# Performance work log

Measured on AMD Instinct MI355X. Metric: run time of the kernel, lower is better.

## Reference

```python
import jax, jax.numpy as jnp
import numpy as np

N_NODES = 50000
N_EDGES = 800000
D_IN = 256
D_OUT = 128
EPS = 1e-9


def setup_inputs() -> dict:
    key = jax.random.key(0)
    ks = jax.random.split(key, 6)
    feat = jax.random.normal(ks[0], (N_NODES, D_IN), dtype=jnp.float32)
    edge_row = jax.random.randint(ks[1], (N_EDGES,), 0, N_NODES)
    edge_col = jax.random.randint(ks[2], (N_EDGES,), 0, N_NODES)
    # normalized adjacency values (positive, ~1/degree scale)
    edge_val = jax.random.uniform(ks[3], (N_EDGES,), dtype=jnp.float32) / 16.0
    # xavier_uniform for Linear(dim_in, dim_out) weights, stored as [D_IN, D_OUT]
    limit = float(np.sqrt(6.0 / (D_IN + D_OUT)))
    W0 = jax.random.uniform(ks[4], (D_IN, D_OUT), minval=-limit, maxval=limit, dtype=jnp.float32)
    W1 = jax.random.uniform(ks[5], (D_IN, D_OUT), minval=-limit, maxval=limit, dtype=jnp.float32)
    zeros = jnp.zeros((D_OUT,), dtype=jnp.float32)
    ones = jnp.ones((D_OUT,), dtype=jnp.float32)
    return {
        "feat": feat,
        "W0": W0, "b0": zeros, "scale0": ones, "offset0": zeros,
        "W1": W1, "b1": zeros, "scale1": ones, "offset1": zeros,
        "edge_row": edge_row, "edge_col": edge_col, "edge_val": edge_val,
    }


def _spmm(edge_row, edge_col, edge_val, x):
    # out[r] += val * x[c] for each edge (r, c, val)  -- sparse adj @ x
    msgs = edge_val[:, None] * x[edge_col]  # [E, D]
    return jax.ops.segment_sum(msgs, edge_row, num_segments=N_NODES)


def _feat_trans(x, W, b, scale, offset):
    h = jax.nn.relu(x @ W + b)  # [N, D_OUT]
    mean = jnp.mean(h, axis=1, keepdims=True)
    var = jnp.var(h, axis=1, keepdims=True) + EPS  # unbiased=False (population var)
    return (h - mean) * scale * jax.lax.rsqrt(var) + offset


def reference(feat, W0, b0, scale0, offset0, W1, b1, scale1, offset1,
              edge_row, edge_col, edge_val):
    # non-first-layer path: feat_hop = [X, A @ X] (order=1), dropout p=0 is identity
    hop1 = _spmm(edge_row, edge_col, edge_val, feat)
    f0 = _feat_trans(feat, W0, b0, scale0, offset0)
    f1 = _feat_trans(hop1, W1, b1, scale1, offset1)
    return jnp.concatenate([f0, f1], axis=1)  # aggr == 'concat'
```

## Files before the change

### kernel.cpp

```cpp
#include <hip/hip_runtime.h>

#define N_NODES 50000
#define N_EDGES 800000
#define D_IN    256
#define D_OUT   128
#define EPS     1e-9f
#define BPAD    136

#define SCATTER_BLOCKS 196
#define GEMM_MBLKS     391

#define RPB    64
#define NBUCK  782
#define BCAP   1344
#define GSTR   16
#define LCAP   1792

#define SORT_OFF  0
#define HIST_OFF  32768
#define LOFF_OFF  35896
#define BASE_OFF  39024
#define CSUM_OFF  42152
#define CBAS_OFF  42216
#define SMEM_BYTES 42280

typedef __attribute__((ext_vector_type(8))) short bf16x8;
typedef __attribute__((ext_vector_type(4))) float floatx4;

__device__ __forceinline__ ushort f2bf(float x) {
    unsigned u = __float_as_uint(x);
    u += 0x7fffu + ((u >> 16) & 1u);
    return (ushort)(u >> 16);
}

__device__ __forceinline__ bf16x8 packbf(float4 a, float4 b) {
    union { ushort us[8]; bf16x8 v; } r;
    r.us[0] = f2bf(a.x); r.us[1] = f2bf(a.y);
    r.us[2] = f2bf(a.z); r.us[3] = f2bf(a.w);
    r.us[4] = f2bf(b.x); r.us[5] = f2bf(b.y);
    r.us[6] = f2bf(b.z); r.us[7] = f2bf(b.w);
    return r.v;
}

#define WB_BLOCKS  32
__global__ __launch_bounds__(256) void prep_small(
    const float* __restrict__ W0, const float* __restrict__ W1,
    ushort* __restrict__ Wb, int* __restrict__ gcnt)
{
    int bid = blockIdx.x;
    int t   = threadIdx.x;
    if (bid == 0) {
        for (int i = t; i < NBUCK * GSTR; i += 256) gcnt[i] = 0;
    } else {
        int g  = (bid - 1) * 256 + t;
        int n  = g >> 5;
        int kq = g & 31;
        const float* W = (n < 128) ? W0 : W1;
        int nn = n & 127;
        union { ushort us[8]; uint4 v; } tmp;
#pragma unroll
        for (int j = 0; j < 8; ++j)
            tmp.us[j] = f2bf(W[(size_t)(kq * 8 + j) * D_OUT + nn]);
        *(uint4*)&Wb[(size_t)n * D_IN + kq * 8] = tmp.v;
    }
}

__global__ __launch_bounds__(512, 4) void gemm_scatter(
    const float* __restrict__ feat, const ushort* __restrict__ Wb,
    const float* __restrict__ bias, const float* __restrict__ scale,
    const float* __restrict__ offset,
    float* __restrict__ out, ushort* __restrict__ Y1,
    const int* __restrict__ er, const int* __restrict__ ec,
    const float* __restrict__ ev, int* __restrict__ gcnt,
    uint2* __restrict__ bedge)
{
    __shared__ __align__(16) char smem[SMEM_BYTES];

    const int t = threadIdx.x;

    if (blockIdx.x < SCATTER_BLOCKS) {
        uint2* sorted = (uint2*)(smem + SORT_OFF);
        int*   hist   = (int*)(smem + HIST_OFF);
        int*   loff   = (int*)(smem + LOFF_OFF);
        int*   base   = (int*)(smem + BASE_OFF);
        int*   csum   = (int*)(smem + CSUM_OFF);
        int*   cbas   = (int*)(smem + CBAS_OFF);

        for (int i = t; i < NBUCK; i += 512) hist[i] = 0;
        __syncthreads();

        const int ebase  = blockIdx.x * 4096;
        const int ecount = min(4096, N_EDGES - ebase);
        int   bkt[8], rnk[8];
        uint2 pk[8];
#pragma unroll
        for (int u = 0; u < 8; ++u) {
            int e = ebase + u * 512 + t;
            bool ok = (e < N_EDGES);
            int   r = ok ? er[e] : 0;
            int   c = ok ? ec[e] : 0;
            float v = ok ? ev[e] : 0.f;
            int   b = r >> 6;
            bkt[u] = ok ? b : -1;
            pk[u]  = make_uint2(((unsigned)b << 22) |
                                ((unsigned)(r & 63) << 16) | (unsigned)c,
                                __float_as_uint(v));
            if (ok) rnk[u] = atomicAdd(&hist[b], 1);
        }
        __syncthreads();

        {
            const int lane = t & 63, w = t >> 6;
            int v0 = (t < NBUCK) ? hist[t] : 0;
            int x0 = v0;
#pragma unroll
            for (int s = 1; s < 64; s <<= 1) {
                int y = __shfl_up(x0, s);
                if (lane >= s) x0 += y;
            }
            if (lane == 63) csum[w] = x0;
            const int i1 = t + 512;
            int v1 = (i1 < NBUCK) ? hist[i1] : 0;
            int x1 = v1;
#pragma unroll
            for (int s = 1; s < 64; s <<= 1) {
                int y = __shfl_up(x1, s);
                if (lane >= s) x1 += y;
            }
            if (lane == 63) csum[8 + w] = x1;
            __syncthreads();
            if (t == 0) {
                int run = 0;
#pragma unroll
                for (int c = 0; c < 16; ++c) { cbas[c] = run; run += csum[c]; }
            }
            __syncthreads();
            if (t < NBUCK)  loff[t]  = x0 - v0 + cbas[w];
            if (i1 < NBUCK) loff[i1] = x1 - v1 + cbas[8 + w];
        }
        __syncthreads();

#pragma unroll
        for (int u = 0; u < 8; ++u) {
            if (bkt[u] >= 0)
                sorted[loff[bkt[u]] + rnk[u]] = pk[u];
        }
        for (int i = t; i < NBUCK; i += 512) {
            int h = hist[i];
            base[i] = h ? atomicAdd(&gcnt[i * GSTR], h) : 0;
        }
        __syncthreads();

#pragma unroll
        for (int u = 0; u < 8; ++u) {
            int k = t + u * 512;
            if (k < ecount) {
                uint2 e = sorted[k];
                int b   = (int)(e.x >> 22);
                int pos = base[b] + (k - loff[b]);
                if (pos < BCAP)
                    bedge[(size_t)b * BCAP + pos] = e;
            }
        }
        return;
    }

    const int gbid = blockIdx.x - SCATTER_BLOCKS;
    const int half = gbid / GEMM_MBLKS;
    const int mblk = gbid % GEMM_MBLKS;
    const int wave = t >> 6, lane = t & 63;
    const int quad = lane >> 4, l16 = lane & 15;
    const int m0   = mblk * 128;
    const int n0   = half * 128;
    ushort* Bs = (ushort*)smem;

    const int grow = m0 + wave * 16 + l16;
    const int arow = grow < N_NODES ? grow : 0;
    const float* aptr = &feat[(size_t)arow * D_IN + quad * 8];

    floatx4 acc[8];
#pragma unroll
    for (int nt = 0; nt < 8; ++nt)
        acc[nt] = (floatx4){0.f, 0.f, 0.f, 0.f};

    for (int kt = 0; kt < D_IN; kt += 128) {
#pragma unroll
        for (int i = 0; i < 8; ++i) {
            int g = t + i * 512;
            int row = g >> 4, kq = g & 15;
            *(uint4*)&Bs[row * BPAD + kq * 8] =
                *(const uint4*)&Wb[(size_t)(n0 + row) * D_IN + kt + kq * 8];
        }
        __syncthreads();

        const float* p = aptr + kt;
        float4 q0 = *(const float4*)(p +  0), q1 = *(const float4*)(p +  4);
        float4 q2 = *(const float4*)(p + 32), q3 = *(const float4*)(p + 36);
        float4 q4 = *(const float4*)(p + 64), q5 = *(const float4*)(p + 68);
        float4 q6 = *(const float4*)(p + 96), q7 = *(const float4*)(p + 100);
        bf16x8 a0 = packbf(q0, q1), a1 = packbf(q2, q3);
        bf16x8 a2 = packbf(q4, q5), a3 = packbf(q6, q7);

#pragma unroll
        for (int s = 0; s < 4; ++s) {
            bf16x8 a = (s == 0) ? a0 : (s == 1) ? a1 : (s == 2) ? a2 : a3;
            const int kk = s * 32;
            bf16x8 b[8];
#pragma unroll
            for (int nt = 0; nt < 8; ++nt)
                b[nt] = *(bf16x8*)&Bs[(nt * 16 + l16) * BPAD + kk + quad * 8];
#pragma unroll
            for (int nt = 0; nt < 8; ++nt)
                acc[nt] = __builtin_amdgcn_mfma_f32_16x16x32_bf16(
                    a, b[nt], acc[nt], 0, 0, 0);
        }
        __syncthreads();
    }

    if (half == 0) {
        float bb[8], sc[8], of[8];
#pragma unroll
        for (int nt = 0; nt < 8; ++nt) {
            bb[nt] = bias[nt * 16 + l16];
            sc[nt] = scale[nt * 16 + l16];
            of[nt] = offset[nt * 16 + l16];
        }
#pragma unroll
        for (int i = 0; i < 4; ++i) {
            float h[8], s = 0.f, q = 0.f;
#pragma unroll
            for (int nt = 0; nt < 8; ++nt) {
                h[nt] = fmaxf(acc[nt][i] + bb[nt], 0.f);
                s += h[nt];
                q += h[nt] * h[nt];
            }
#pragma unroll
            for (int m = 1; m < 16; m <<= 1) {
                s += __shfl_xor(s, m);
                q += __shfl_xor(q, m);
            }
            float mean = s * (1.f / 128.f);
            float inv  = rsqrtf(q * (1.f / 128.f) - mean * mean + EPS);
            int row = m0 + wave * 16 + quad * 4 + i;
            if (row < N_NODES) {
#pragma unroll
                for (int nt = 0; nt < 8; ++nt)
                    out[(size_t)row * 256 + nt * 16 + l16] =
                        (h[nt] - mean) * sc[nt] * inv + of[nt];
            }
        }
    } else {
#pragma unroll
        for (int i = 0; i < 4; ++i) {
            int row = m0 + wave * 16 + quad * 4 + i;
            if (row < N_NODES) {
#pragma unroll
                for (int nt = 0; nt < 8; ++nt)
                    Y1[(size_t)row * D_OUT + nt * 16 + l16] =
                        f2bf(acc[nt][i]);
            }
        }
    }
}

__global__ __launch_bounds__(512) void spmm_csr_ln(
    const int* __restrict__ gcnt, const uint2* __restrict__ bedge,
    const ushort* __restrict__ Y,
    const float* __restrict__ bias, const float* __restrict__ scale,
    const float* __restrict__ offset, float* __restrict__ out)
{
    __shared__ uint2 lds_e[LCAP];
    __shared__ int   cnt[RPB];
    __shared__ int   offx[RPB];
    __shared__ int   cntp[RPB];

    const int t      = threadIdx.x;
    const int bucket = blockIdx.x;
    const int r0     = bucket * RPB;
    const int nrows  = min(RPB, N_NODES - r0);
    int ne = gcnt[bucket * GSTR];
    ne = ne < BCAP ? ne : BCAP;

    if (t < RPB) cnt[t] = 0;
    {
        uint4* ez = (uint4*)lds_e;
        ez[t] = make_uint4(0u, 0u, 0u, 0u);
        if (t + 512 < 896) ez[t + 512] = make_uint4(0u, 0u, 0u, 0u);
    }
    __syncthreads();

    const size_t base = (size_t)bucket * BCAP;
    int   erA = -1, erB = -1, erC = -1;
    unsigned exA = 0, exB = 0, exC = 0;
    unsigned evA = 0, evB = 0, evC = 0;
    int   rkA = 0,  rkB = 0,  rkC = 0;
    if (t < ne) {
        uint2 p = bedge[base + t];
        erA = (int)((p.x >> 16) & 63u); exA = (p.x & 0xffffu) << 8;
        evA = p.y;
        rkA = atomicAdd(&cnt[erA], 1);
    }
    if (t + 512 < ne) {
        uint2 p = bedge[base + t + 512];
        erB = (int)((p.x >> 16) & 63u); exB = (p.x & 0xffffu) << 8;
        evB = p.y;
        rkB = atomicAdd(&cnt[erB], 1);
    }
    if (t + 1024 < ne) {
        uint2 p = bedge[base + t + 1024];
        erC = (int)((p.x >> 16) & 63u); exC = (p.x & 0xffffu) << 8;
        evC = p.y;
        rkC = atomicAdd(&cnt[erC], 1);
    }
    __syncthreads();

    if (t < RPB) {
        int c  = cnt[t];
        int cp = (c + 7) & ~7;
        int x  = cp;
#pragma unroll
        for (int s = 1; s < RPB; s <<= 1) {
            int w = __shfl_up(x, s);
            if (t >= s) x += w;
        }
        offx[t] = x - cp;
        cntp[t] = cp;
    }
    __syncthreads();

    if (erA >= 0) lds_e[offx[erA] + rkA] = make_uint2(exA, evA);
    if (erB >= 0) lds_e[offx[erB] + rkB] = make_uint2(exB, evB);
    if (erC >= 0) lds_e[offx[erC] + rkC] = make_uint2(exC, evC);
    __syncthreads();

    const int wave  = t >> 6, lane = t & 63;
    const int lane4 = lane * 4;
    const int cidx  = lane * 2;
    const char* Yb  = (const char*)Y;
    const float b0v = bias[cidx],   b1v = bias[cidx + 1];
    const float s0v = scale[cidx],  s1v = scale[cidx + 1];
    const float o0v = offset[cidx], o1v = offset[cidx + 1];

    for (int ri = wave; ri < nrows; ri += 8) {
        int beg = offx[ri], np = cntp[ri];
        float ax = 0.f, ay = 0.f;
        for (int j = 0; j < np; j += 8) {
            uint2 e[8];
#pragma unroll
            for (int u = 0; u < 8; ++u)
                e[u] = lds_e[beg + j + u];
            unsigned yv[8];
#pragma unroll
            for (int u = 0; u < 8; ++u)
                yv[u] = *(const unsigned*)(Yb + e[u].x + lane4);
#pragma unroll
            for (int u = 0; u < 8; ++u) {
                float v = __uint_as_float(e[u].y);
                ax = fmaf(v, __uint_as_float(yv[u] << 16), ax);
                ay = fmaf(v, __uint_as_float(yv[u] & 0xffff0000u), ay);
            }
        }
        float h0 = fmaxf(ax + b0v, 0.f);
        float h1 = fmaxf(ay + b1v, 0.f);
        float s = h0 + h1, q = h0 * h0 + h1 * h1;
#pragma unroll
        for (int m = 1; m < 64; m <<= 1) {
            s += __shfl_xor(s, m);
            q += __shfl_xor(q, m);
        }
        float mean = s * (1.f / 128.f);
        float inv  = rsqrtf(q * (1.f / 128.f) - mean * mean + EPS);
        int row = r0 + ri;
        float2 o;
        o.x = (h0 - mean) * s0v * inv + o0v;
        o.y = (h1 - mean) * s1v * inv + o1v;
        *(float2*)&out[(size_t)row * 256 + 128 + cidx] = o;
    }
}

extern "C" void kernel_launch(void* const* d_in, const int* in_sizes, int n_in,
                              void* d_out, int out_size, void* d_ws, size_t ws_size,
                              hipStream_t stream)
{
    const float* feat = (const float*)d_in[0];
    const float* W0   = (const float*)d_in[1];
    const float* b0   = (const float*)d_in[2];
    const float* s0   = (const float*)d_in[3];
    const float* o0   = (const float*)d_in[4];
    const float* W1   = (const float*)d_in[5];
    const float* b1   = (const float*)d_in[6];
    const float* s1   = (const float*)d_in[7];
    const float* o1   = (const float*)d_in[8];
    const int*   er   = (const int*)d_in[9];
    const int*   ec   = (const int*)d_in[10];
    const float* ev   = (const float*)d_in[11];
    float* out = (float*)d_out;

    char*   wsb   = (char*)d_ws;
    ushort* Wb    = (ushort*)(wsb);
    ushort* Y1    = (ushort*)(wsb + 131072);
    int*    gcnt  = (int*)   (wsb + 12931072);
    uint2*  bedge = (uint2*) (wsb + 12981248);

    prep_small<<<1 + WB_BLOCKS, 256, 0, stream>>>(W0, W1, Wb, gcnt);

    gemm_scatter<<<SCATTER_BLOCKS + 2 * GEMM_MBLKS, 512, 0, stream>>>(
        feat, Wb, b0, s0, o0, out, Y1, er, ec, ev, gcnt, bedge);

    spmm_csr_ln<<<NBUCK, 512, 0, stream>>>(
        gcnt, bedge, Y1, b1, s1, o1, out);
}
```

Before: 173.9 us.

## Compute both weight halves per GEMM block to reuse feature loads

Each GEMM block now computes all 256 output columns (W0 and W1 halves) for its 128 rows instead of splitting the two halves across separate blocks. The K loop is retiled to 64-wide steps with a smaller LDS stride so both weight halves fit in shared memory. This halves the number of GEMM blocks and stops each feature row from being read and converted to bf16 twice. In exchange, accumulator registers double, which can lower occupancy, and each block carries more serial work.

New measurement: 178.5 us. +2.7%, slower.

```diff
diff --git a/kernel.cpp b/kernel.cpp
--- a/kernel.cpp
+++ b/kernel.cpp
@@ -5,7 +5,7 @@
 #define D_IN    256
 #define D_OUT   128
 #define EPS     1e-9f
-#define BPAD    136
+#define BSTR    72
 
 #define SCATTER_BLOCKS 196
 #define GEMM_MBLKS     391
@@ -165,59 +165,60 @@
         return;
     }
 
-    const int gbid = blockIdx.x - SCATTER_BLOCKS;
-    const int half = gbid / GEMM_MBLKS;
-    const int mblk = gbid % GEMM_MBLKS;
+    const int mblk = blockIdx.x - SCATTER_BLOCKS;
     const int wave = t >> 6, lane = t & 63;
     const int quad = lane >> 4, l16 = lane & 15;
     const int m0   = mblk * 128;
-    const int n0   = half * 128;
     ushort* Bs = (ushort*)smem;
 
     const int grow = m0 + wave * 16 + l16;
     const int arow = grow < N_NODES ? grow : 0;
     const float* aptr = &feat[(size_t)arow * D_IN + quad * 8];
 
-    floatx4 acc[8];
-#pragma unroll
-    for (int nt = 0; nt < 8; ++nt)
+    floatx4 acc[16];
+#pragma unroll
+    for (int nt = 0; nt < 16; ++nt)
         acc[nt] = (floatx4){0.f, 0.f, 0.f, 0.f};
 
-    for (int kt = 0; kt < D_IN; kt += 128) {
-#pragma unroll
-        for (int i = 0; i < 8; ++i) {
+    for (int kt = 0; kt < D_IN; kt += 64) {
+#pragma unroll
+        for (int i = 0; i < 4; ++i) {
             int g = t + i * 512;
-            int row = g >> 4, kq = g & 15;
-            *(uint4*)&Bs[row * BPAD + kq * 8] =
-                *(const uint4*)&Wb[(size_t)(n0 + row) * D_IN + kt + kq * 8];
+            int row = g >> 3, kq = g & 7;
+            *(uint4*)&Bs[row * BSTR + kq * 8] =
+                *(const uint4*)&Wb[(size_t)row * D_IN + kt + kq * 8];
         }
         __syncthreads();
 
         const float* p = aptr + kt;
         float4 q0 = *(const float4*)(p +  0), q1 = *(const float4*)(p +  4);
         float4 q2 = *(const float4*)(p + 32), q3 = *(const float4*)(p + 36);
-        float4 q4 = *(const float4*)(p + 64), q5 = *(const float4*)(p + 68);
-        float4 q6 = *(const float4*)(p + 96), q7 = *(const float4*)(p + 100);
         bf16x8 a0 = packbf(q0, q1), a1 = packbf(q2, q3);
-        bf16x8 a2 = packbf(q4, q5), a3 = packbf(q6, q7);
-
-#pragma unroll
-        for (int s = 0; s < 4; ++s) {
-            bf16x8 a = (s == 0) ? a0 : (s == 1) ? a1 : (s == 2) ? a2 : a3;
+
+#pragma unroll
+        for (int s = 0; s < 2; ++s) {
+            bf16x8 a = s ? a1 : a0;
             const int kk = s * 32;
             bf16x8 b[8];
 #pragma unroll
             for (int nt = 0; nt < 8; ++nt)
-                b[nt] = *(bf16x8*)&Bs[(nt * 16 + l16) * BPAD + kk + quad * 8];
+                b[nt] = *(bf16x8*)&Bs[(nt * 16 + l16) * BSTR + kk + quad * 8];
 #pragma unroll
             for (int nt = 0; nt < 8; ++nt)
                 acc[nt] = __builtin_amdgcn_mfma_f32_16x16x32_bf16(
                     a, b[nt], acc[nt], 0, 0, 0);
-        }
-        __syncthreads();
-    }
-
-    if (half == 0) {
+#pragma unroll
+            for (int nt = 0; nt < 8; ++nt)
+                b[nt] = *(bf16x8*)&Bs[(128 + nt * 16 + l16) * BSTR + kk + quad * 8];
+#pragma unroll
+            for (int nt = 0; nt < 8; ++nt)
+                acc[8 + nt] = __builtin_amdgcn_mfma_f32_16x16x32_bf16(
+                    a, b[nt], acc[8 + nt], 0, 0, 0);
+        }
+        __syncthreads();
+    }
+
+    {
         float bb[8], sc[8], of[8];
 #pragma unroll
         for (int nt = 0; nt < 8; ++nt) {
@@ -247,17 +248,10 @@
                 for (int nt = 0; nt < 8; ++nt)
                     out[(size_t)row * 256 + nt * 16 + l16] =
                         (h[nt] - mean) * sc[nt] * inv + of[nt];
-            }
-        }
-    } else {
-#pragma unroll
-        for (int i = 0; i < 4; ++i) {
-            int row = m0 + wave * 16 + quad * 4 + i;
-            if (row < N_NODES) {
 #pragma unroll
                 for (int nt = 0; nt < 8; ++nt)
                     Y1[(size_t)row * D_OUT + nt * 16 + l16] =
-                        f2bf(acc[nt][i]);
+                        f2bf(acc[8 + nt][i]);
             }
         }
     }
@@ -404,7 +398,7 @@
 
     prep_small<<<1 + WB_BLOCKS, 256, 0, stream>>>(W0, W1, Wb, gcnt);
 
-    gemm_scatter<<<SCATTER_BLOCKS + 2 * GEMM_MBLKS, 512, 0, stream>>>(
+    gemm_scatter<<<SCATTER_BLOCKS + GEMM_MBLKS, 512, 0, stream>>>(
         feat, Wb, b0, s0, o0, out, Y1, er, ec, ev, gcnt, bedge);
 
     spmm_csr_ln<<<NBUCK, 512, 0, stream>>>(
```

## Drop local edge sort in scatter and shrink GEMM LDS tile for occupancy

Applied to the files above, without the earlier changes.

The scatter blocks no longer sort edges in shared memory by bucket. Each thread now writes its edges straight to the global bucket array at base plus its atomic rank, which removes the prefix scan, the sorted staging buffer and several barriers. The GEMM staging of the B tile moves from two 128-wide K phases to four 64-wide phases with a narrower stride, cutting shared memory from about 42KB to about 18.5KB so more blocks can be resident. The cost is scattered, less coalesced global writes for edges and more barriers per K loop in the GEMM.

Measured after the change: 178.9 us. +2.9%, slower.

```diff
diff --git a/kernel.cpp b/kernel.cpp
--- a/kernel.cpp
+++ b/kernel.cpp
@@ -5,7 +5,7 @@
 #define D_IN    256
 #define D_OUT   128
 #define EPS     1e-9f
-#define BPAD    136
+#define BSTR    72
 
 #define SCATTER_BLOCKS 196
 #define GEMM_MBLKS     391
@@ -16,13 +16,9 @@
 #define GSTR   16
 #define LCAP   1792
 
-#define SORT_OFF  0
-#define HIST_OFF  32768
-#define LOFF_OFF  35896
-#define BASE_OFF  39024
-#define CSUM_OFF  42152
-#define CBAS_OFF  42216
-#define SMEM_BYTES 42280
+#define HIST_OFF  0
+#define BASE_OFF  3200
+#define SMEM_BYTES 18560
 
 typedef __attribute__((ext_vector_type(8))) short bf16x8;
 typedef __attribute__((ext_vector_type(4))) float floatx4;
@@ -79,18 +75,12 @@
     const int t = threadIdx.x;
 
     if (blockIdx.x < SCATTER_BLOCKS) {
-        uint2* sorted = (uint2*)(smem + SORT_OFF);
-        int*   hist   = (int*)(smem + HIST_OFF);
-        int*   loff   = (int*)(smem + LOFF_OFF);
-        int*   base   = (int*)(smem + BASE_OFF);
-        int*   csum   = (int*)(smem + CSUM_OFF);
-        int*   cbas   = (int*)(smem + CBAS_OFF);
-
+        int* hist = (int*)(smem + HIST_OFF);
+        int* base = (int*)(smem + BASE_OFF);
         for (int i = t; i < NBUCK; i += 512) hist[i] = 0;
         __syncthreads();
 
-        const int ebase  = blockIdx.x * 4096;
-        const int ecount = min(4096, N_EDGES - ebase);
+        int ebase = blockIdx.x * 4096;
         int   bkt[8], rnk[8];
         uint2 pk[8];
 #pragma unroll
@@ -100,66 +90,23 @@
             int   r = ok ? er[e] : 0;
             int   c = ok ? ec[e] : 0;
             float v = ok ? ev[e] : 0.f;
-            int   b = r >> 6;
-            bkt[u] = ok ? b : -1;
-            pk[u]  = make_uint2(((unsigned)b << 22) |
-                                ((unsigned)(r & 63) << 16) | (unsigned)c,
+            bkt[u] = ok ? (r >> 6) : -1;
+            pk[u]  = make_uint2(((unsigned)(r & 63) << 16) | (unsigned)c,
                                 __float_as_uint(v));
-            if (ok) rnk[u] = atomicAdd(&hist[b], 1);
-        }
-        __syncthreads();
-
-        {
-            const int lane = t & 63, w = t >> 6;
-            int v0 = (t < NBUCK) ? hist[t] : 0;
-            int x0 = v0;
-#pragma unroll
-            for (int s = 1; s < 64; s <<= 1) {
-                int y = __shfl_up(x0, s);
-                if (lane >= s) x0 += y;
-            }
-            if (lane == 63) csum[w] = x0;
-            const int i1 = t + 512;
-            int v1 = (i1 < NBUCK) ? hist[i1] : 0;
-            int x1 = v1;
-#pragma unroll
-            for (int s = 1; s < 64; s <<= 1) {
-                int y = __shfl_up(x1, s);
-                if (lane >= s) x1 += y;
-            }
-            if (lane == 63) csum[8 + w] = x1;
-            __syncthreads();
-            if (t == 0) {
-                int run = 0;
-#pragma unroll
-                for (int c = 0; c < 16; ++c) { cbas[c] = run; run += csum[c]; }
-            }
-            __syncthreads();
-            if (t < NBUCK)  loff[t]  = x0 - v0 + cbas[w];
-            if (i1 < NBUCK) loff[i1] = x1 - v1 + cbas[8 + w];
-        }
-        __syncthreads();
-
-#pragma unroll
-        for (int u = 0; u < 8; ++u) {
-            if (bkt[u] >= 0)
-                sorted[loff[bkt[u]] + rnk[u]] = pk[u];
-        }
+            if (ok) rnk[u] = atomicAdd(&hist[r >> 6], 1);
+        }
+        __syncthreads();
         for (int i = t; i < NBUCK; i += 512) {
             int h = hist[i];
             base[i] = h ? atomicAdd(&gcnt[i * GSTR], h) : 0;
         }
         __syncthreads();
-
 #pragma unroll
         for (int u = 0; u < 8; ++u) {
-            int k = t + u * 512;
-            if (k < ecount) {
-                uint2 e = sorted[k];
-                int b   = (int)(e.x >> 22);
-                int pos = base[b] + (k - loff[b]);
+            if (bkt[u] >= 0) {
+                int pos = base[bkt[u]] + rnk[u];
                 if (pos < BCAP)
-                    bedge[(size_t)b * BCAP + pos] = e;
+                    bedge[(size_t)bkt[u] * BCAP + pos] = pk[u];
             }
         }
         return;
@@ -183,12 +130,14 @@
     for (int nt = 0; nt < 8; ++nt)
         acc[nt] = (floatx4){0.f, 0.f, 0.f, 0.f};
 
-    for (int kt = 0; kt < D_IN; kt += 128) {
-#pragma unroll
-        for (int i = 0; i < 8; ++i) {
+#pragma unroll
+    for (int ph = 0; ph < 4; ++ph) {
+        const int kt = ph * 64;
+#pragma unroll
+        for (int i = 0; i < 2; ++i) {
             int g = t + i * 512;
-            int row = g >> 4, kq = g & 15;
-            *(uint4*)&Bs[row * BPAD + kq * 8] =
+            int row = g >> 3, kq = g & 7;
+            *(uint4*)&Bs[row * BSTR + kq * 8] =
                 *(const uint4*)&Wb[(size_t)(n0 + row) * D_IN + kt + kq * 8];
         }
         __syncthreads();
@@ -196,23 +145,20 @@
         const float* p = aptr + kt;
         float4 q0 = *(const float4*)(p +  0), q1 = *(const float4*)(p +  4);
         float4 q2 = *(const float4*)(p + 32), q3 = *(const float4*)(p + 36);
-        float4 q4 = *(const float4*)(p + 64), q5 = *(const float4*)(p + 68);
-        float4 q6 = *(const float4*)(p + 96), q7 = *(const float4*)(p + 100);
         bf16x8 a0 = packbf(q0, q1), a1 = packbf(q2, q3);
-        bf16x8 a2 = packbf(q4, q5), a3 = packbf(q6, q7);
-
-#pragma unroll
-        for (int s = 0; s < 4; ++s) {
-            bf16x8 a = (s == 0) ? a0 : (s == 1) ? a1 : (s == 2) ? a2 : a3;
+
+#pragma unroll
+        for (int s = 0; s < 2; ++s) {
+            bf16x8 av = s ? a1 : a0;
             const int kk = s * 32;
             bf16x8 b[8];
 #pragma unroll
             for (int nt = 0; nt < 8; ++nt)
-                b[nt] = *(bf16x8*)&Bs[(nt * 16 + l16) * BPAD + kk + quad * 8];
+                b[nt] = *(bf16x8*)&Bs[(nt * 16 + l16) * BSTR + kk + quad * 8];
 #pragma unroll
             for (int nt = 0; nt < 8; ++nt)
                 acc[nt] = __builtin_amdgcn_mfma_f32_16x16x32_bf16(
-                    a, b[nt], acc[nt], 0, 0, 0);
+                    av, b[nt], acc[nt], 0, 0, 0);
         }
         __syncthreads();
     }
```
